# Kernel optimization log

Measured on AMD Instinct MI355X. Metric: run time of the kernel, lower is better.

The kernel has to match this reference:

```python
import jax, jax.numpy as jnp
import numpy as np


def setup_inputs() -> dict:
    key = jax.random.key(0)
    k_x, k_b = jax.random.split(key)
    B, C, H, W = 32, 512, 32, 32
    x = jax.random.normal(k_x, (B, C, H, W), dtype=jnp.float32)
    beta = jax.random.normal(k_b, (1,), dtype=jnp.float32)
    return {"x": x, "beta": beta}


def reference(x, beta):
    B, C, H, W = x.shape
    feat = x.reshape(B, C, H * W)                       # [B, C, N]
    # channel-channel Gram matrix: [B, C, C]
    attn = jnp.einsum('bcn,bdn->bcd', feat, feat)
    # DANet-style reversed scores: rowmax - score, then softmax over last dim
    attn = jnp.max(attn, axis=-1, keepdims=True) - attn
    attn = jax.nn.softmax(attn, axis=-1)
    feat_e = jnp.einsum('bcd,bdn->bcn', attn, feat).reshape(B, C, H, W)
    return beta * feat_e + x
```

## Files before the change

kernel.cpp:

```cpp
#include <hip/hip_runtime.h>
#include <math.h>

constexpr int B = 32, C = 512, N = 1024;

typedef float f32x4 __attribute__((ext_vector_type(4)));
typedef _Float16 f16x8 __attribute__((ext_vector_type(8)));
typedef unsigned short u16x4 __attribute__((ext_vector_type(4)));
typedef unsigned short u16x8 __attribute__((ext_vector_type(8)));

__device__ __forceinline__ unsigned short f32_to_f16u(float v) {
  union { _Float16 h; unsigned short u; } cv; cv.h = (_Float16)v; return cv.u;
}
__device__ __forceinline__ float f16u_to_f32(unsigned short u) {
  union { _Float16 h; unsigned short u; } cv; cv.u = u; return (float)cv.h;
}

__device__ __forceinline__ void glds16(const void* g, void* l) {
  __builtin_amdgcn_global_load_lds((const __attribute__((address_space(1))) void*)g,
                                   (__attribute__((address_space(3))) void*)l, 16, 0, 0);
}

__global__ __launch_bounds__(256) void convert_kernel(const float* __restrict__ x,
                                                      unsigned short* __restrict__ xf,
                                                      unsigned short* __restrict__ xfT) {
  const int b = blockIdx.z;
  const int cy = blockIdx.y * 64;
  const int nx = blockIdx.x * 64;
  const int t = threadIdx.x;
  const int r = t >> 4, c4 = (t & 15) * 4;

  __shared__ unsigned T[64][65];

#pragma unroll
  for (int rr = 0; rr < 64; rr += 16) {
    const int row = rr + r;
    const size_t gi = ((size_t)b * C + cy + row) * N + nx + c4;
    const float4 v = *(const float4*)&x[gi];
    u16x4 h;
    h[0] = f32_to_f16u(v.x); h[1] = f32_to_f16u(v.y);
    h[2] = f32_to_f16u(v.z); h[3] = f32_to_f16u(v.w);
    *(u16x4*)&xf[gi] = h;
    T[row][c4 + 0] = h[0]; T[row][c4 + 1] = h[1];
    T[row][c4 + 2] = h[2]; T[row][c4 + 3] = h[3];
  }
  __syncthreads();
#pragma unroll
  for (int rr = 0; rr < 64; rr += 16) {
    const int nrow = rr + r;
    u16x4 o;
    o[0] = (unsigned short)T[c4 + 0][nrow]; o[1] = (unsigned short)T[c4 + 1][nrow];
    o[2] = (unsigned short)T[c4 + 2][nrow]; o[3] = (unsigned short)T[c4 + 3][nrow];
    *(u16x4*)&xfT[((size_t)b * N + nx + nrow) * C + cy + c4] = o;
  }
}

__global__ __launch_bounds__(1024, 4) void gram_soft_av(const unsigned short* __restrict__ xf,
                                                        const unsigned short* __restrict__ xfT,
                                                        const float* __restrict__ beta,
                                                        float* __restrict__ out) {
  const int l = blockIdx.x;
  const int xcd = l & 7, seq = l >> 3;
  const int b = xcd + 8 * (seq >> 3);
  const int i0 = (seq & 7) * 64;

  const unsigned short* __restrict__ Fh = xf  + (size_t)b * C * N;
  const unsigned short* __restrict__ FT = xfT + (size_t)b * N * C;
  float* __restrict__ ob = out + (size_t)b * C * N;

  __shared__ __align__(16) unsigned short Pb[4][512 * 32];
  unsigned short* Atile = &Pb[2][0];

  const int t = threadIdx.x, wave = t >> 6, lane = t & 63;
  const int wi = wave >> 3;
  const int wj = wave & 7;
  const int lrow = lane & 15, quad = lane >> 4;
  const int srow = lane >> 2;
  const int sel  = ((lane & 3) ^ ((lane >> 3) & 3)) * 8;

  f32x4 acc[2][4] = {};

#define STAGE1(k0, nb)                                                    \
  {                                                                       \
    _Pragma("unroll")                                                     \
    for (int cc = 0; cc < 2; ++cc) {                                      \
      const int chunk = wave * 2 + cc;                                    \
      const int row = chunk * 16 + srow;                                  \
      glds16(Fh + (size_t)row * N + (k0) + sel, &Pb[nb][chunk * 512]);    \
    }                                                                     \
  }

  STAGE1(0, 0);
  STAGE1(32, 1);
  STAGE1(64, 2);

  for (int it = 0; it < 32; ++it) {
    const int k0 = it * 32;
    if (it < 30)       asm volatile("s_waitcnt vmcnt(4)" ::: "memory");
    else if (it == 30) asm volatile("s_waitcnt vmcnt(2)" ::: "memory");
    else               asm volatile("s_waitcnt vmcnt(0)" ::: "memory");
    __builtin_amdgcn_s_barrier();
    if (it + 3 < 32) STAGE1(k0 + 96, (it + 3) & 3);

    const unsigned short* __restrict__ Pc = Pb[it & 3];
    f16x8 ah[2], bh[4];
#pragma unroll
    for (int ti = 0; ti < 2; ++ti) {
      const int r = i0 + wi * 32 + ti * 16 + lrow;
      ah[ti] = *(const f16x8*)&Pc[r * 32 + (quad ^ ((r >> 1) & 3)) * 8];
    }
#pragma unroll
    for (int tj = 0; tj < 4; ++tj) {
      const int r = wj * 64 + tj * 16 + lrow;
      bh[tj] = *(const f16x8*)&Pc[r * 32 + (quad ^ ((r >> 1) & 3)) * 8];
    }
#pragma unroll
    for (int ti = 0; ti < 2; ++ti)
#pragma unroll
      for (int tj = 0; tj < 4; ++tj)
        acc[ti][tj] = __builtin_amdgcn_mfma_f32_16x16x32_f16(ah[ti], bh[tj], acc[ti][tj], 0, 0, 0);
  }
#undef STAGE1

  __syncthreads();
  float* red = (float*)&Pb[0][0];
  float* fin = red + 512;

  float m[8];
#pragma unroll
  for (int ti = 0; ti < 2; ++ti)
#pragma unroll
    for (int rr = 0; rr < 4; ++rr)
      m[ti * 4 + rr] = fminf(fminf(acc[ti][0][rr], acc[ti][1][rr]),
                             fminf(acc[ti][2][rr], acc[ti][3][rr]));
#pragma unroll
  for (int o = 1; o < 16; o <<= 1)
#pragma unroll
    for (int s = 0; s < 8; ++s) m[s] = fminf(m[s], __shfl_xor(m[s], o, 64));
  if (lrow == 0)
#pragma unroll
    for (int ti = 0; ti < 2; ++ti)
#pragma unroll
      for (int rr = 0; rr < 4; ++rr)
        red[wave * 32 + ti * 16 + quad * 4 + rr] = m[ti * 4 + rr];
  __syncthreads();
  if (t < 64) {
    const int wig = t >> 5, loc = t & 31;
    float v = red[(wig * 8) * 32 + loc];
#pragma unroll
    for (int j = 1; j < 8; ++j) v = fminf(v, red[(wig * 8 + j) * 32 + loc]);
    fin[t] = v;
  }
  __syncthreads();

  float sm[8];
#pragma unroll
  for (int ti = 0; ti < 2; ++ti)
#pragma unroll
    for (int rr = 0; rr < 4; ++rr) {
      const float mn = fin[wi * 32 + ti * 16 + quad * 4 + rr];
      float s = 0.f;
#pragma unroll
      for (int tj = 0; tj < 4; ++tj) {
        const float e = __expf(mn - acc[ti][tj][rr]);
        acc[ti][tj][rr] = e;
        s += e;
      }
      sm[ti * 4 + rr] = s;
    }
#pragma unroll
  for (int o = 1; o < 16; o <<= 1)
#pragma unroll
    for (int s = 0; s < 8; ++s) sm[s] += __shfl_xor(sm[s], o, 64);
  if (lrow == 0)
#pragma unroll
    for (int ti = 0; ti < 2; ++ti)
#pragma unroll
      for (int rr = 0; rr < 4; ++rr)
        red[wave * 32 + ti * 16 + quad * 4 + rr] = sm[ti * 4 + rr];
  __syncthreads();
  if (t < 64) {
    const int wig = t >> 5, loc = t & 31;
    float v = 0.f;
#pragma unroll
    for (int j = 0; j < 8; ++j) v += red[(wig * 8 + j) * 32 + loc];
    fin[t] = 1.0f / v;
  }
  __syncthreads();

#pragma unroll
  for (int ti = 0; ti < 2; ++ti)
#pragma unroll
    for (int rr = 0; rr < 4; ++rr) {
      const float inv = fin[wi * 32 + ti * 16 + quad * 4 + rr];
      const int rl = wi * 32 + ti * 16 + quad * 4 + rr;
#pragma unroll
      for (int tj = 0; tj < 4; ++tj) {
        const int gcol = wj * 64 + tj * 16 + lrow;
        Atile[rl * 512 + ((((gcol >> 3) ^ (rl & 7)) << 3) | (gcol & 7))] =
            f32_to_f16u(acc[ti][tj][rr] * inv);
      }
    }
  __syncthreads();

  const float bv = beta[0];

  for (int jp = 0; jp < 2; ++jp) {
    f32x4 eacc[2][4] = {};
    u16x8 rsA[2];
#define LOADR_E(k0)                                                            \
    {                                                                          \
      _Pragma("unroll")                                                        \
      for (int cc = 0; cc < 2; ++cc) {                                         \
        const int chunk = wave * 2 + cc;                                       \
        const int row = chunk * 16 + srow;                                     \
        rsA[cc] = *(const u16x8*)&FT[(size_t)(jp * 512 + row) * C + (k0) + sel]; \
      }                                                                        \
    }
#define WRITER_E(nb)                                                           \
    {                                                                          \
      _Pragma("unroll")                                                        \
      for (int cc = 0; cc < 2; ++cc) {                                         \
        const int chunk = wave * 2 + cc;                                       \
        *(u16x8*)&Pb[nb][chunk * 512 + lane * 8] = rsA[cc];                    \
      }                                                                        \
    }
    LOADR_E(0);
    WRITER_E(0);
    LOADR_E(32);
    asm volatile("s_waitcnt lgkmcnt(0)" ::: "memory");
    __builtin_amdgcn_s_barrier();

    for (int it = 0; it < 16; ++it) {
      const int k0 = it * 32;
      const unsigned short* __restrict__ Pc = Pb[it & 1];
      f16x8 ah[2], bh[4];
#pragma unroll
      for (int ti = 0; ti < 2; ++ti) {
        const int ra = wi * 32 + ti * 16 + lrow;
        ah[ti] = *(const f16x8*)&Atile[ra * 512 + ((((k0 >> 3) | quad) ^ (ra & 7)) << 3)];
      }
#pragma unroll
      for (int tj = 0; tj < 4; ++tj) {
        const int rb = wj * 64 + tj * 16 + lrow;
        bh[tj] = *(const f16x8*)&Pc[rb * 32 + ((quad ^ ((rb >> 1) & 3)) << 3)];
      }
#pragma unroll
      for (int ti = 0; ti < 2; ++ti)
#pragma unroll
        for (int tj = 0; tj < 4; ++tj)
          eacc[ti][tj] = __builtin_amdgcn_mfma_f32_16x16x32_f16(ah[ti], bh[tj], eacc[ti][tj], 0, 0, 0);

      if (it + 1 < 16) WRITER_E((it + 1) & 1);
      if (it + 2 < 16) LOADR_E(k0 + 64);
      asm volatile("s_waitcnt lgkmcnt(0)" ::: "memory");
      __builtin_amdgcn_s_barrier();
    }
#undef LOADR_E
#undef WRITER_E

    float* fs = (float*)&Pb[0][0] + wave * 1024;
#pragma unroll
    for (int ti = 0; ti < 2; ++ti) {
#pragma unroll
      for (int tj = 0; tj < 4; ++tj)
#pragma unroll
        for (int r = 0; r < 4; ++r)
          fs[(quad * 4 + r) * 64 + tj * 16 + lrow] = eacc[ti][tj][r];
      __syncthreads();
#pragma unroll
      for (int p = 0; p < 4; ++p) {
        const int f = p * 64 + lane;
        const int rr2 = f >> 4, cc4 = (f & 15) * 4;
        const f32x4 e = *(const f32x4*)&fs[rr2 * 64 + cc4];
        const int gr = i0 + wi * 32 + ti * 16 + rr2;
        const int gc = jp * 512 + wj * 64 + cc4;
        const size_t o = (size_t)gr * N + gc;
        const u16x4 xv = *(const u16x4*)&Fh[o];
        f32x4 ov;
        ov[0] = fmaf(bv, e[0], f16u_to_f32(xv[0]));
        ov[1] = fmaf(bv, e[1], f16u_to_f32(xv[1]));
        ov[2] = fmaf(bv, e[2], f16u_to_f32(xv[2]));
        ov[3] = fmaf(bv, e[3], f16u_to_f32(xv[3]));
        __builtin_nontemporal_store(ov, (f32x4*)&ob[o]);
      }
      __syncthreads();
    }
  }
}

extern "C" void kernel_launch(void* const* d_in, const int* in_sizes, int n_in,
                              void* d_out, int out_size, void* d_ws, size_t ws_size,
                              hipStream_t stream) {
  const float* x    = (const float*)d_in[0];
  const float* beta = (const float*)d_in[1];
  float* out = (float*)d_out;

  char* ws = (char*)d_ws;
  unsigned short* xf  = (unsigned short*)ws; ws += (size_t)B * C * N * 2;
  unsigned short* xfT = (unsigned short*)ws;

  convert_kernel<<<dim3(N / 64, C / 64, B), dim3(256),  0, stream>>>(x, xf, xfT);
  gram_soft_av  <<<dim3(256),               dim3(1024), 0, stream>>>(xf, xfT, beta, out);
}
```

Baseline: 177.4 us.

## Halve block to 512 threads with 64x64 per-wave tiles and MFMA priority

Switches the fused gram/softmax/AV kernel from 16 waves to 8 waves per block. Each wave now covers all 64 rows and a 64-column strip, which doubles per-wave accumulators and fragment reuse and cuts LDS fragment reads per MFMA. MFMA loops are wrapped in s_setprio, and the epilogue's block-wide barriers are replaced by a per-wave lgkmcnt wait, since each wave now uses its own scratch region. The cost is roughly doubled register pressure per wave and fewer waves available to hide memory latency.

```diff
diff --git a/kernel.cpp b/kernel.cpp
--- a/kernel.cpp
+++ b/kernel.cpp
@@ -54,10 +54,10 @@
   }
 }
 
-__global__ __launch_bounds__(1024, 4) void gram_soft_av(const unsigned short* __restrict__ xf,
-                                                        const unsigned short* __restrict__ xfT,
-                                                        const float* __restrict__ beta,
-                                                        float* __restrict__ out) {
+__global__ __launch_bounds__(512, 2) void gram_soft_av(const unsigned short* __restrict__ xf,
+                                                       const unsigned short* __restrict__ xfT,
+                                                       const float* __restrict__ beta,
+                                                       float* __restrict__ out) {
   const int l = blockIdx.x;
   const int xcd = l & 7, seq = l >> 3;
   const int b = xcd + 8 * (seq >> 3);
@@ -71,19 +71,17 @@
   unsigned short* Atile = &Pb[2][0];
 
   const int t = threadIdx.x, wave = t >> 6, lane = t & 63;
-  const int wi = wave >> 3;
-  const int wj = wave & 7;
   const int lrow = lane & 15, quad = lane >> 4;
   const int srow = lane >> 2;
   const int sel  = ((lane & 3) ^ ((lane >> 3) & 3)) * 8;
 
-  f32x4 acc[2][4] = {};
+  f32x4 acc[4][4] = {};
 
 #define STAGE1(k0, nb)                                                    \
   {                                                                       \
     _Pragma("unroll")                                                     \
-    for (int cc = 0; cc < 2; ++cc) {                                      \
-      const int chunk = wave * 2 + cc;                                    \
+    for (int cc = 0; cc < 4; ++cc) {                                      \
+      const int chunk = wave * 4 + cc;                                    \
       const int row = chunk * 16 + srow;                                  \
       glds16(Fh + (size_t)row * N + (k0) + sel, &Pb[nb][chunk * 512]);    \
     }                                                                     \
@@ -95,29 +93,31 @@
 
   for (int it = 0; it < 32; ++it) {
     const int k0 = it * 32;
-    if (it < 30)       asm volatile("s_waitcnt vmcnt(4)" ::: "memory");
-    else if (it == 30) asm volatile("s_waitcnt vmcnt(2)" ::: "memory");
+    if (it < 30)       asm volatile("s_waitcnt vmcnt(8)" ::: "memory");
+    else if (it == 30) asm volatile("s_waitcnt vmcnt(4)" ::: "memory");
     else               asm volatile("s_waitcnt vmcnt(0)" ::: "memory");
     __builtin_amdgcn_s_barrier();
     if (it + 3 < 32) STAGE1(k0 + 96, (it + 3) & 3);
 
     const unsigned short* __restrict__ Pc = Pb[it & 3];
-    f16x8 ah[2], bh[4];
-#pragma unroll
-    for (int ti = 0; ti < 2; ++ti) {
-      const int r = i0 + wi * 32 + ti * 16 + lrow;
+    f16x8 ah[4], bh[4];
+#pragma unroll
+    for (int ti = 0; ti < 4; ++ti) {
+      const int r = i0 + ti * 16 + lrow;
       ah[ti] = *(const f16x8*)&Pc[r * 32 + (quad ^ ((r >> 1) & 3)) * 8];
     }
 #pragma unroll
     for (int tj = 0; tj < 4; ++tj) {
-      const int r = wj * 64 + tj * 16 + lrow;
+      const int r = wave * 64 + tj * 16 + lrow;
       bh[tj] = *(const f16x8*)&Pc[r * 32 + (quad ^ ((r >> 1) & 3)) * 8];
     }
-#pragma unroll
-    for (int ti = 0; ti < 2; ++ti)
+    __builtin_amdgcn_s_setprio(1);
+#pragma unroll
+    for (int ti = 0; ti < 4; ++ti)
 #pragma unroll
       for (int tj = 0; tj < 4; ++tj)
         acc[ti][tj] = __builtin_amdgcn_mfma_f32_16x16x32_f16(ah[ti], bh[tj], acc[ti][tj], 0, 0, 0);
+    __builtin_amdgcn_s_setprio(0);
   }
 #undef STAGE1
 
@@ -125,9 +125,9 @@
   float* red = (float*)&Pb[0][0];
   float* fin = red + 512;
 
-  float m[8];
-#pragma unroll
-  for (int ti = 0; ti < 2; ++ti)
+  float m[16];
+#pragma unroll
+  for (int ti = 0; ti < 4; ++ti)
 #pragma unroll
     for (int rr = 0; rr < 4; ++rr)
       m[ti * 4 + rr] = fminf(fminf(acc[ti][0][rr], acc[ti][1][rr]),
@@ -135,29 +135,28 @@
 #pragma unroll
   for (int o = 1; o < 16; o <<= 1)
 #pragma unroll
-    for (int s = 0; s < 8; ++s) m[s] = fminf(m[s], __shfl_xor(m[s], o, 64));
+    for (int s = 0; s < 16; ++s) m[s] = fminf(m[s], __shfl_xor(m[s], o, 64));
   if (lrow == 0)
 #pragma unroll
-    for (int ti = 0; ti < 2; ++ti)
+    for (int ti = 0; ti < 4; ++ti)
 #pragma unroll
       for (int rr = 0; rr < 4; ++rr)
-        red[wave * 32 + ti * 16 + quad * 4 + rr] = m[ti * 4 + rr];
+        red[wave * 64 + ti * 16 + quad * 4 + rr] = m[ti * 4 + rr];
   __syncthreads();
   if (t < 64) {
-    const int wig = t >> 5, loc = t & 31;
-    float v = red[(wig * 8) * 32 + loc];
-#pragma unroll
-    for (int j = 1; j < 8; ++j) v = fminf(v, red[(wig * 8 + j) * 32 + loc]);
+    float v = red[t];
+#pragma unroll
+    for (int j = 1; j < 8; ++j) v = fminf(v, red[j * 64 + t]);
     fin[t] = v;
   }
   __syncthreads();
 
-  float sm[8];
-#pragma unroll
-  for (int ti = 0; ti < 2; ++ti)
+  float sm[16];
+#pragma unroll
+  for (int ti = 0; ti < 4; ++ti)
 #pragma unroll
     for (int rr = 0; rr < 4; ++rr) {
-      const float mn = fin[wi * 32 + ti * 16 + quad * 4 + rr];
+      const float mn = fin[ti * 16 + quad * 4 + rr];
       float s = 0.f;
 #pragma unroll
       for (int tj = 0; tj < 4; ++tj) {
@@ -170,32 +169,31 @@
 #pragma unroll
   for (int o = 1; o < 16; o <<= 1)
 #pragma unroll
-    for (int s = 0; s < 8; ++s) sm[s] += __shfl_xor(sm[s], o, 64);
+    for (int s = 0; s < 16; ++s) sm[s] += __shfl_xor(sm[s], o, 64);
   if (lrow == 0)
 #pragma unroll
-    for (int ti = 0; ti < 2; ++ti)
+    for (int ti = 0; ti < 4; ++ti)
 #pragma unroll
       for (int rr = 0; rr < 4; ++rr)
-        red[wave * 32 + ti * 16 + quad * 4 + rr] = sm[ti * 4 + rr];
+        red[wave * 64 + ti * 16 + quad * 4 + rr] = sm[ti * 4 + rr];
   __syncthreads();
   if (t < 64) {
-    const int wig = t >> 5, loc = t & 31;
     float v = 0.f;
 #pragma unroll
-    for (int j = 0; j < 8; ++j) v += red[(wig * 8 + j) * 32 + loc];
+    for (int j = 0; j < 8; ++j) v += red[j * 64 + t];
     fin[t] = 1.0f / v;
   }
   __syncthreads();
 
 #pragma unroll
-  for (int ti = 0; ti < 2; ++ti)
+  for (int ti = 0; ti < 4; ++ti)
 #pragma unroll
     for (int rr = 0; rr < 4; ++rr) {
-      const float inv = fin[wi * 32 + ti * 16 + quad * 4 + rr];
-      const int rl = wi * 32 + ti * 16 + quad * 4 + rr;
+      const float inv = fin[ti * 16 + quad * 4 + rr];
+      const int rl = ti * 16 + quad * 4 + rr;
 #pragma unroll
       for (int tj = 0; tj < 4; ++tj) {
-        const int gcol = wj * 64 + tj * 16 + lrow;
+        const int gcol = wave * 64 + tj * 16 + lrow;
         Atile[rl * 512 + ((((gcol >> 3) ^ (rl & 7)) << 3) | (gcol & 7))] =
             f32_to_f16u(acc[ti][tj][rr] * inv);
       }
@@ -205,13 +203,13 @@
   const float bv = beta[0];
 
   for (int jp = 0; jp < 2; ++jp) {
-    f32x4 eacc[2][4] = {};
-    u16x8 rsA[2];
+    f32x4 eacc[4][4] = {};
+    u16x8 rsA[4];
 #define LOADR_E(k0)                                                            \
     {                                                                          \
       _Pragma("unroll")                                                        \
-      for (int cc = 0; cc < 2; ++cc) {                                         \
-        const int chunk = wave * 2 + cc;                                       \
+      for (int cc = 0; cc < 4; ++cc) {                                         \
+        const int chunk = wave * 4 + cc;                                       \
         const int row = chunk * 16 + srow;                                     \
         rsA[cc] = *(const u16x8*)&FT[(size_t)(jp * 512 + row) * C + (k0) + sel]; \
       }                                                                        \
@@ -219,8 +217,8 @@
 #define WRITER_E(nb)                                                           \
     {                                                                          \
       _Pragma("unroll")                                                        \
-      for (int cc = 0; cc < 2; ++cc) {                                         \
-        const int chunk = wave * 2 + cc;                                       \
+      for (int cc = 0; cc < 4; ++cc) {                                         \
+        const int chunk = wave * 4 + cc;                                       \
         *(u16x8*)&Pb[nb][chunk * 512 + lane * 8] = rsA[cc];                    \
       }                                                                        \
     }
@@ -233,22 +231,24 @@
     for (int it = 0; it < 16; ++it) {
       const int k0 = it * 32;
       const unsigned short* __restrict__ Pc = Pb[it & 1];
-      f16x8 ah[2], bh[4];
-#pragma unroll
-      for (int ti = 0; ti < 2; ++ti) {
-        const int ra = wi * 32 + ti * 16 + lrow;
-        ah[ti] = *(const f16x8*)&Atile[ra * 512 + ((((k0 >> 3) | quad) ^ (ra & 7)) << 3)];
+      f16x8 ah[4], bh[4];
+#pragma unroll
+      for (int ti = 0; ti < 4; ++ti) {
+        const int ra = ti * 16 + lrow;
+        ah[ti] = *(const f16x8*)&Atile[ra * 512 + ((((k0 >> 3) + quad) ^ (ra & 7)) << 3)];
       }
 #pragma unroll
       for (int tj = 0; tj < 4; ++tj) {
-        const int rb = wj * 64 + tj * 16 + lrow;
+        const int rb = wave * 64 + tj * 16 + lrow;
         bh[tj] = *(const f16x8*)&Pc[rb * 32 + ((quad ^ ((rb >> 1) & 3)) << 3)];
       }
-#pragma unroll
-      for (int ti = 0; ti < 2; ++ti)
+      __builtin_amdgcn_s_setprio(1);
+#pragma unroll
+      for (int ti = 0; ti < 4; ++ti)
 #pragma unroll
         for (int tj = 0; tj < 4; ++tj)
           eacc[ti][tj] = __builtin_amdgcn_mfma_f32_16x16x32_f16(ah[ti], bh[tj], eacc[ti][tj], 0, 0, 0);
+      __builtin_amdgcn_s_setprio(0);
 
       if (it + 1 < 16) WRITER_E((it + 1) & 1);
       if (it + 2 < 16) LOADR_E(k0 + 64);
@@ -260,20 +260,20 @@
 
     float* fs = (float*)&Pb[0][0] + wave * 1024;
 #pragma unroll
-    for (int ti = 0; ti < 2; ++ti) {
+    for (int ti = 0; ti < 4; ++ti) {
 #pragma unroll
       for (int tj = 0; tj < 4; ++tj)
 #pragma unroll
         for (int r = 0; r < 4; ++r)
           fs[(quad * 4 + r) * 64 + tj * 16 + lrow] = eacc[ti][tj][r];
-      __syncthreads();
+      asm volatile("s_waitcnt lgkmcnt(0)" ::: "memory");
 #pragma unroll
       for (int p = 0; p < 4; ++p) {
         const int f = p * 64 + lane;
         const int rr2 = f >> 4, cc4 = (f & 15) * 4;
         const f32x4 e = *(const f32x4*)&fs[rr2 * 64 + cc4];
-        const int gr = i0 + wi * 32 + ti * 16 + rr2;
-        const int gc = jp * 512 + wj * 64 + cc4;
+        const int gr = i0 + ti * 16 + rr2;
+        const int gc = jp * 512 + wave * 64 + cc4;
         const size_t o = (size_t)gr * N + gc;
         const u16x4 xv = *(const u16x4*)&Fh[o];
         f32x4 ov;
@@ -283,7 +283,6 @@
         ov[3] = fmaf(bv, e[3], f16u_to_f32(xv[3]));
         __builtin_nontemporal_store(ov, (f32x4*)&ob[o]);
       }
-      __syncthreads();
     }
   }
 }
@@ -299,6 +298,6 @@
   unsigned short* xf  = (unsigned short*)ws; ws += (size_t)B * C * N * 2;
   unsigned short* xfT = (unsigned short*)ws;
 
-  convert_kernel<<<dim3(N / 64, C / 64, B), dim3(256),  0, stream>>>(x, xf, xfT);
-  gram_soft_av  <<<dim3(256),               dim3(1024), 0, stream>>>(xf, xfT, beta, out);
-}
+  convert_kernel<<<dim3(N / 64, C / 64, B), dim3(256), 0, stream>>>(x, xf, xfT);
+  gram_soft_av  <<<dim3(256),               dim3(512), 0, stream>>>(xf, xfT, beta, out);
+}
```

New measurement: 174.9 us. Within noise of the previous version (-1.4%).
